# Optimization experiments

Hardware: AMD Instinct MI355X
Metric: run time of the kernel (lower is better)

The kernel has to match this reference:

```python
import jax, jax.numpy as jnp
import numpy as np

NUM_FRAMES = 10000
NR = 2_000_000


def _vec2skew(v):
    # Faithful to ExtrinsicsLearner.vec2skew: columns are s0,s1,s2 (stack along dim=2).
    zero = jnp.zeros_like(v[:, 0])
    s0 = jnp.stack([zero, -v[:, 2], v[:, 1]], axis=1)   # (nr, 3)
    s1 = jnp.stack([v[:, 2], zero, -v[:, 0]], axis=1)
    s2 = jnp.stack([-v[:, 1], v[:, 0], zero], axis=1)
    return jnp.stack([s0, s1, s2], axis=2)              # (nr, 3, 3)


def _exp_so3(r):
    # Rodrigues formula, matching Exp(): eps added to norm, not norm^2 clamped.
    skew = _vec2skew(r)                                  # (nr, 3, 3)
    n = jnp.linalg.norm(r, axis=1) + 1e-15               # (nr,)
    eye = jnp.eye(3, dtype=r.dtype)
    a = (jnp.sin(n) / n)[:, None, None]
    b = ((1.0 - jnp.cos(n)) / (n * n))[:, None, None]
    return eye[None] + a * skew + b * (skew @ skew)


def setup_inputs() -> dict:
    key = jax.random.key(0)
    k1, k2, k3, k4, k5 = jax.random.split(key, 5)
    # Learned per-frame pose corrections (small, as after a few optim steps)
    r = jax.random.normal(k1, (NUM_FRAMES, 3), dtype=jnp.float32) * 0.05
    t = jax.random.normal(k2, (NUM_FRAMES, 3), dtype=jnp.float32) * 0.05
    # Initial extrinsics: valid rigid transforms (R0 | t0; 0 0 0 1)
    r0 = jax.random.normal(k3, (NUM_FRAMES, 3), dtype=jnp.float32) * 0.5
    R0 = _exp_so3(r0)                                    # (N, 3, 3)
    t0 = jax.random.normal(k4, (NUM_FRAMES, 3, 1), dtype=jnp.float32)
    top = jnp.concatenate([R0, t0], axis=2)              # (N, 3, 4)
    bottom = jnp.broadcast_to(
        jnp.array([[0.0, 0.0, 0.0, 1.0]], dtype=jnp.float32), (NUM_FRAMES, 1, 4))
    initial_extrinsics = jnp.concatenate([top, bottom], axis=1)  # (N, 4, 4)
    cam_id = jax.random.randint(k5, (NR,), 0, NUM_FRAMES, dtype=jnp.int64)
    return {"r": r, "t": t, "initial_extrinsics": initial_extrinsics,
            "cam_id": cam_id}


def reference(r, t, initial_extrinsics, cam_id):
    rg = r[cam_id]                                       # (nr, 3) gather
    tg = t[cam_id]                                       # (nr, 3)
    R = _exp_so3(rg)                                     # (nr, 3, 3)
    c2w34 = jnp.concatenate([R, tg[:, :, None]], axis=2)  # (nr, 3, 4)
    bottom = jnp.broadcast_to(
        jnp.array([[0.0, 0.0, 0.0, 1.0]], dtype=c2w34.dtype), (rg.shape[0], 1, 4))
    c2w = jnp.concatenate([c2w34, bottom], axis=1)       # (nr, 4, 4)
    extrinsics = jnp.linalg.inv(c2w)                     # batched 4x4 inverse
    return initial_extrinsics[cam_id] @ extrinsics       # (nr, 4, 4)
```

## Files before the change

### kernel.cpp

```cpp
#include <hip/hip_runtime.h>

typedef float f32x4 __attribute__((ext_vector_type(4)));

__device__ __forceinline__ void compute_M(float rx, float ry, float rz,
                                          float tx, float ty, float tz,
                                          const float* __restrict__ E,
                                          f32x4* __restrict__ Mout) {
    float s = rx * rx + ry * ry + rz * rz;
    float n = sqrtf(s) + 1e-15f;
    float sn = sinf(n), cn = cosf(n);
    float A = sn / n;
    float B = (1.0f - cn) / (n * n);

    float R00 = 1.0f + B * (rx * rx - s);
    float R01 =  A * rz + B * (rx * ry);
    float R02 = -A * ry + B * (rx * rz);
    float R10 = -A * rz + B * (rx * ry);
    float R11 = 1.0f + B * (ry * ry - s);
    float R12 =  A * rx + B * (ry * rz);
    float R20 =  A * ry + B * (rx * rz);
    float R21 = -A * rx + B * (ry * rz);
    float R22 = 1.0f + B * (rz * rz - s);

    float T00 = R00, T01 = R10, T02 = R20;
    float T10 = R01, T11 = R11, T12 = R21;
    float T20 = R02, T21 = R12, T22 = R22;
    float u0 = -(T00 * tx + T01 * ty + T02 * tz);
    float u1 = -(T10 * tx + T11 * ty + T12 * tz);
    float u2 = -(T20 * tx + T21 * ty + T22 * tz);

    #pragma unroll
    for (int i = 0; i < 4; ++i) {
        float e0 = E[4 * i + 0], e1 = E[4 * i + 1];
        float e2 = E[4 * i + 2], e3 = E[4 * i + 3];
        f32x4 m;
        m.x = e0 * T00 + e1 * T10 + e2 * T20;
        m.y = e0 * T01 + e1 * T11 + e2 * T21;
        m.z = e0 * T02 + e1 * T12 + e2 * T22;
        m.w = e0 * u0 + e1 * u1 + e2 * u2 + e3;
        Mout[i] = m;
    }
}

__global__ void build_table_kernel(const float* __restrict__ r,
                                   const float* __restrict__ t,
                                   const float* __restrict__ e0,
                                   float* __restrict__ M, int nf) {
    int f = blockIdx.x * blockDim.x + threadIdx.x;
    if (f >= nf) return;
    f32x4 m[4];
    compute_M(r[3 * f + 0], r[3 * f + 1], r[3 * f + 2],
              t[3 * f + 0], t[3 * f + 1], t[3 * f + 2],
              e0 + 16 * f, m);
    f32x4* Mo = reinterpret_cast<f32x4*>(M + 16 * f);
    Mo[0] = m[0]; Mo[1] = m[1]; Mo[2] = m[2]; Mo[3] = m[3];
}

__global__ void gather_kernel(const int* __restrict__ cid,
                              const f32x4* __restrict__ M,
                              f32x4* __restrict__ out, int n4) {
    int tid = blockIdx.x * blockDim.x + threadIdx.x;
    if (tid >= n4) return;
    int ray = tid >> 2;
    int c = tid & 3;
    int cam = __builtin_nontemporal_load(cid + ray);
    f32x4 v = M[cam * 4 + c];
    __builtin_nontemporal_store(v, out + tid);
}

__global__ void fused_kernel(const float* __restrict__ r,
                             const float* __restrict__ t,
                             const float* __restrict__ e0,
                             const int* __restrict__ cid,
                             f32x4* __restrict__ out, int nr) {
    int ray = blockIdx.x * blockDim.x + threadIdx.x;
    if (ray >= nr) return;
    int f = cid[ray];
    f32x4 m[4];
    compute_M(r[3 * f + 0], r[3 * f + 1], r[3 * f + 2],
              t[3 * f + 0], t[3 * f + 1], t[3 * f + 2],
              e0 + 16 * f, m);
    __builtin_nontemporal_store(m[0], out + ray * 4 + 0);
    __builtin_nontemporal_store(m[1], out + ray * 4 + 1);
    __builtin_nontemporal_store(m[2], out + ray * 4 + 2);
    __builtin_nontemporal_store(m[3], out + ray * 4 + 3);
}

extern "C" void kernel_launch(void* const* d_in, const int* in_sizes, int n_in,
                              void* d_out, int out_size, void* d_ws, size_t ws_size,
                              hipStream_t stream) {
    const float* r  = (const float*)d_in[0];
    const float* t  = (const float*)d_in[1];
    const float* e0 = (const float*)d_in[2];
    const int*  cid = (const int*)d_in[3];
    float* out = (float*)d_out;

    const int nf = in_sizes[0] / 3;
    const int nr = in_sizes[3];
    const size_t table_bytes = (size_t)nf * 16 * sizeof(float);

    if (ws_size >= table_bytes) {
        float* M = (float*)d_ws;
        {
            int threads = 256;
            int blocks = (nf + threads - 1) / threads;
            build_table_kernel<<<blocks, threads, 0, stream>>>(r, t, e0, M, nf);
        }
        {
            int n4 = nr * 4;
            int threads = 256;
            int blocks = (n4 + threads - 1) / threads;
            gather_kernel<<<blocks, threads, 0, stream>>>(
                cid, (const f32x4*)M, (f32x4*)out, n4);
        }
    } else {
        int threads = 256;
        int blocks = (nr + threads - 1) / threads;
        fused_kernel<<<blocks, threads, 0, stream>>>(
            r, t, e0, cid, (f32x4*)out, nr);
    }
}
```

Measured before the change: 159.7 us.

## Always use fused per-ray kernel instead of table build plus gather

Removes the two-kernel path that built a per-frame transform table in workspace and then gathered it per ray. Every ray now recomputes the Rodrigues rotation, inverse and product directly from the per-frame inputs in a single kernel. This drops one launch and the table round-trip, but repeats transcendental work per ray. The output stores also change from nontemporal to ordinary vector stores, and launch bounds are added.

Result: slower. 178.7 us (+11.9%).

```diff
diff --git a/kernel.cpp b/kernel.cpp
--- a/kernel.cpp
+++ b/kernel.cpp
@@ -42,37 +42,12 @@
     }
 }
 
-__global__ void build_table_kernel(const float* __restrict__ r,
-                                   const float* __restrict__ t,
-                                   const float* __restrict__ e0,
-                                   float* __restrict__ M, int nf) {
-    int f = blockIdx.x * blockDim.x + threadIdx.x;
-    if (f >= nf) return;
-    f32x4 m[4];
-    compute_M(r[3 * f + 0], r[3 * f + 1], r[3 * f + 2],
-              t[3 * f + 0], t[3 * f + 1], t[3 * f + 2],
-              e0 + 16 * f, m);
-    f32x4* Mo = reinterpret_cast<f32x4*>(M + 16 * f);
-    Mo[0] = m[0]; Mo[1] = m[1]; Mo[2] = m[2]; Mo[3] = m[3];
-}
-
-__global__ void gather_kernel(const int* __restrict__ cid,
-                              const f32x4* __restrict__ M,
-                              f32x4* __restrict__ out, int n4) {
-    int tid = blockIdx.x * blockDim.x + threadIdx.x;
-    if (tid >= n4) return;
-    int ray = tid >> 2;
-    int c = tid & 3;
-    int cam = __builtin_nontemporal_load(cid + ray);
-    f32x4 v = M[cam * 4 + c];
-    __builtin_nontemporal_store(v, out + tid);
-}
-
-__global__ void fused_kernel(const float* __restrict__ r,
-                             const float* __restrict__ t,
-                             const float* __restrict__ e0,
-                             const int* __restrict__ cid,
-                             f32x4* __restrict__ out, int nr) {
+__global__ __launch_bounds__(256) void fused_kernel(
+        const float* __restrict__ r,
+        const float* __restrict__ t,
+        const float* __restrict__ e0,
+        const int* __restrict__ cid,
+        f32x4* __restrict__ out, int nr) {
     int ray = blockIdx.x * blockDim.x + threadIdx.x;
     if (ray >= nr) return;
     int f = cid[ray];
@@ -80,10 +55,11 @@
     compute_M(r[3 * f + 0], r[3 * f + 1], r[3 * f + 2],
               t[3 * f + 0], t[3 * f + 1], t[3 * f + 2],
               e0 + 16 * f, m);
-    __builtin_nontemporal_store(m[0], out + ray * 4 + 0);
-    __builtin_nontemporal_store(m[1], out + ray * 4 + 1);
-    __builtin_nontemporal_store(m[2], out + ray * 4 + 2);
-    __builtin_nontemporal_store(m[3], out + ray * 4 + 3);
+    f32x4* o = out + (size_t)ray * 4;
+    o[0] = m[0];
+    o[1] = m[1];
+    o[2] = m[2];
+    o[3] = m[3];
 }
 
 extern "C" void kernel_launch(void* const* d_in, const int* in_sizes, int n_in,
@@ -95,28 +71,9 @@
     const int*  cid = (const int*)d_in[3];
     float* out = (float*)d_out;
 
-    const int nf = in_sizes[0] / 3;
     const int nr = in_sizes[3];
-    const size_t table_bytes = (size_t)nf * 16 * sizeof(float);
-
-    if (ws_size >= table_bytes) {
-        float* M = (float*)d_ws;
-        {
-            int threads = 256;
-            int blocks = (nf + threads - 1) / threads;
-            build_table_kernel<<<blocks, threads, 0, stream>>>(r, t, e0, M, nf);
-        }
-        {
-            int n4 = nr * 4;
-            int threads = 256;
-            int blocks = (n4 + threads - 1) / threads;
-            gather_kernel<<<blocks, threads, 0, stream>>>(
-                cid, (const f32x4*)M, (f32x4*)out, n4);
-        }
-    } else {
-        int threads = 256;
-        int blocks = (nr + threads - 1) / threads;
-        fused_kernel<<<blocks, threads, 0, stream>>>(
-            r, t, e0, cid, (f32x4*)out, nr);
-    }
+    const int threads = 256;
+    const int blocks = (nr + threads - 1) / threads;
+    fused_kernel<<<blocks, threads, 0, stream>>>(
+        r, t, e0, cid, (f32x4*)out, nr);
 }
```
